# Optimization experiments

Measured on AMD Instinct MI355X. Metric: run time of the kernel, lower is better.

Reference implementation:

```python
import jax, jax.numpy as jnp
import numpy as np

NUM_HEADS = 16  # CLIP ViT-L num_attention_heads


def setup_inputs() -> dict:
    key = jax.random.key(0)
    ks = jax.random.split(key, 11)
    B, T, E = 16, 577, 1024
    d = {
        "hidden_states": jax.random.normal(ks[0], (B, T, E), jnp.float32),
        # token 'size' from prior merging steps; sizes are >= 1 in practice
        "size": jax.random.uniform(ks[1], (B, T), jnp.float32) + 1.0,
        "wq": jax.random.normal(ks[2], (E, E), jnp.float32) * (E ** -0.5),
        "bq": jax.random.normal(ks[3], (E,), jnp.float32) * 0.02,
        "wk": jax.random.normal(ks[4], (E, E), jnp.float32) * (E ** -0.5),
        "bk": jax.random.normal(ks[5], (E,), jnp.float32) * 0.02,
        "wv": jax.random.normal(ks[6], (E, E), jnp.float32) * (E ** -0.5),
        "bv": jax.random.normal(ks[7], (E,), jnp.float32) * 0.02,
        "wo": jax.random.normal(ks[8], (E, E), jnp.float32) * (E ** -0.5),
        "bo": jax.random.normal(ks[9], (E,), jnp.float32) * 0.02,
    }
    return d


def reference(hidden_states, size, wq, bq, wk, bk, wv, bv, wo, bo):
    B, T, E = hidden_states.shape
    H = NUM_HEADS
    D = E // H
    scale = D ** -0.5

    # torch nn.Linear: y = x @ W.T + b
    q = (hidden_states @ wq.T + bq) * scale
    k = hidden_states @ wk.T + bk
    v = hidden_states @ wv.T + bv

    def split_heads(x):  # [B,T,E] -> [B,H,T,D]
        return x.reshape(B, T, H, D).transpose(0, 2, 1, 3)

    qh, kh, vh = split_heads(q), split_heads(k), split_heads(v)

    # raw logits (before size bias), [B,H,T,T]
    attn_logits = jnp.einsum("bhtd,bhsd->bhts", qh, kh)

    # att_score: mean over the flattened bsz*num_heads dim, on raw logits
    att_score = attn_logits.mean(axis=(0, 1))  # [T,T]

    # additive log-size bias over keys
    attn_logits = attn_logits + jnp.log(size)[:, None, None, :]

    probs = jax.nn.softmax(attn_logits, axis=-1)  # dropout p=0 / eval
    out = jnp.einsum("bhts,bhsd->bhtd", probs, vh)
    out = out.transpose(0, 2, 1, 3).reshape(B, T, E)
    attn_output = out @ wo.T + bo

    # mean over heads of key states: [B,T,D]
    mean_keys = kh.mean(axis=1)

    return attn_output, mean_keys, att_score
```

## Files before the change

kernel.cpp:

```cpp
#include <hip/hip_runtime.h>
#include <hip/hip_bf16.h>
#include <math.h>

typedef __attribute__((ext_vector_type(8))) short s16x8;
typedef __attribute__((ext_vector_type(4))) short s16x4;
typedef __attribute__((ext_vector_type(4))) float f32x4;
typedef __attribute__((ext_vector_type(8))) __bf16 bf16x8;

#define MFMA16(a, b, c) __builtin_amdgcn_mfma_f32_16x16x32_bf16( \
    __builtin_bit_cast(bf16x8, (a)), __builtin_bit_cast(bf16x8, (b)), (c), 0, 0, 0)

__device__ __forceinline__ short f2b(float f) {
    __bf16 h = (__bf16)f;
    return __builtin_bit_cast(short, h);
}
__device__ __forceinline__ float b2f(short b) {
    union { unsigned u; float f; } x;
    x.u = ((unsigned)(unsigned short)b) << 16;
    return x.f;
}

__device__ __forceinline__ void gload16(const void* g, void* l) {
    __builtin_amdgcn_global_load_lds(
        (const __attribute__((address_space(1))) unsigned int*)g,
        (__attribute__((address_space(3))) unsigned int*)l, 16, 0, 0);
}

__global__ void k_f32_to_bf16(const float* __restrict__ in, short* __restrict__ out, long n) {
    long i = ((long)blockIdx.x * blockDim.x + threadIdx.x) * 4;
    long stride = (long)gridDim.x * blockDim.x * 4;
    for (; i < n; i += stride) {
        float4 v = *(const float4*)(in + i);
        s16x4 o = { f2b(v.x), f2b(v.y), f2b(v.z), f2b(v.w) };
        *(s16x4*)(out + i) = o;
    }
}

__global__ void k_wconv4(const float* __restrict__ w0, const float* __restrict__ w1,
                         const float* __restrict__ w2, const float* __restrict__ w3,
                         short* __restrict__ out, long n) {
    int wsel = blockIdx.y;
    const float* src = (wsel == 0) ? w0 : (wsel == 1) ? w1 : (wsel == 2) ? w2 : w3;
    short* dst = out + (long)wsel * n;
    long i = ((long)blockIdx.x * blockDim.x + threadIdx.x) * 4;
    if (i >= n) return;
    float4 v = *(const float4*)(src + i);
    s16x4 o = { f2b(v.x), f2b(v.y), f2b(v.z), f2b(v.w) };
    *(s16x4*)(dst + i) = o;
}

__global__ void k_sizepad(const float* __restrict__ size, float* __restrict__ out,
                          int B, int T, int SP) {
    int i = blockIdx.x * blockDim.x + threadIdx.x;
    if (i >= B * SP) return;
    int b = i / SP, s = i % SP;
    out[i] = (s < T) ? size[b * T + s] : 0.f;
}

template<bool ROUTE>
__global__ __launch_bounds__(256) void k_gemm4(
    const short* __restrict__ A, const short* __restrict__ Bw,
    const float* __restrict__ bb0, const float* __restrict__ bb1, const float* __restrict__ bb2,
    short* __restrict__ o0, short* __restrict__ o1, short* __restrict__ o2,
    float* __restrict__ Cf, int M, int N, int K, int Ntiles, float alpha0) {

    __shared__ short As[128 * 64];
    __shared__ short Bs[128 * 64];

    int nwg = gridDim.x, orig = blockIdx.x;
    int qq = nwg >> 3, rr = nwg & 7;
    int xcd = orig & 7, pos = orig >> 3;
    int wg = (xcd < rr ? xcd * (qq + 1) : rr * (qq + 1) + (xcd - rr) * qq) + pos;
    int bx = wg % Ntiles, by = wg / Ntiles;
    int row0 = by * 128, col0 = bx * 128;

    int tid = threadIdx.x;
    int lane = tid & 63, wave = tid >> 6;
    int wr = wave >> 1, wc = wave & 1;
    int lr = lane & 15, lg = lane >> 4;

    f32x4 acc[4][4];
    #pragma unroll
    for (int i = 0; i < 4; i++)
        #pragma unroll
        for (int j = 0; j < 4; j++)
            #pragma unroll
            for (int q = 0; q < 4; q++) acc[i][j][q] = 0.f;

    for (int k0 = 0; k0 < K; k0 += 64) {
        __syncthreads();
        #pragma unroll
        for (int i = 0; i < 4; ++i) {
            int cw = i * 256 + wave * 64;
            int c = cw + lane;
            int r = c >> 3;
            int cby = ((c & 7) * 16) ^ ((r & 7) << 4);
            int ra = row0 + r; ra = ra < M ? ra : M - 1;
            gload16((const char*)(A + (long)ra * K + k0) + cby, &As[cw * 8]);
            int rb = col0 + r; rb = rb < N ? rb : N - 1;
            gload16((const char*)(Bw + (long)rb * K + k0) + cby, &Bs[cw * 8]);
        }
        __syncthreads();
        #pragma unroll
        for (int ks = 0; ks < 2; ++ks) {
            s16x8 af[4], bfr[4];
            #pragma unroll
            for (int i = 0; i < 4; ++i) {
                int r = wr * 64 + i * 16 + lr;
                af[i] = *(const s16x8*)((const char*)As + r * 128 +
                        (((ks << 6) + (lg << 4)) ^ ((r & 7) << 4)));
            }
            #pragma unroll
            for (int j = 0; j < 4; ++j) {
                int r = wc * 64 + j * 16 + lr;
                bfr[j] = *(const s16x8*)((const char*)Bs + r * 128 +
                         (((ks << 6) + (lg << 4)) ^ ((r & 7) << 4)));
            }
            #pragma unroll
            for (int i = 0; i < 4; ++i)
                #pragma unroll
                for (int j = 0; j < 4; ++j)
                    acc[i][j] = MFMA16(af[i], bfr[j], acc[i][j]);
        }
    }

    #pragma unroll
    for (int i = 0; i < 4; i++) {
        int grow0 = row0 + wr * 64 + i * 16 + lg * 4;
        #pragma unroll
        for (int j = 0; j < 4; j++) {
            int gc = col0 + wc * 64 + j * 16 + lr;
            if (gc >= N) continue;
            if (ROUTE) {
                int which = gc >> 10, lc = gc & 1023;
                float bias = (which == 0 ? bb0 : which == 1 ? bb1 : bb2)[lc];
                float alpha = (which == 0) ? alpha0 : 1.0f;
                short* op = (which == 0 ? o0 : which == 1 ? o1 : o2);
                #pragma unroll
                for (int q = 0; q < 4; ++q) {
                    int r2 = grow0 + q;
                    if (r2 < M) op[(long)r2 * 1024 + lc] = f2b((acc[i][j][q] + bias) * alpha);
                }
            } else {
                float bias = bb0[gc];
                #pragma unroll
                for (int q = 0; q < 4; ++q) {
                    int r2 = grow0 + q;
                    if (r2 < M) Cf[(long)r2 * N + gc] = acc[i][j][q] + bias;
                }
            }
        }
    }
}

__device__ __forceinline__ void gemm_core(
    const short* __restrict__ Ab, const short* __restrict__ Bb,
    float* __restrict__ Cf, int M, int N, int K, int ldc, int row0, int col0) {
    __shared__ short As[128 * 64];
    __shared__ short Bs[128 * 64];
    int tid = threadIdx.x;
    int lane = tid & 63, wave = tid >> 6;
    int wr = wave >> 1, wc = wave & 1;
    int lr = lane & 15, lg = lane >> 4;
    f32x4 acc[4][4];
    #pragma unroll
    for (int i = 0; i < 4; i++)
        #pragma unroll
        for (int j = 0; j < 4; j++)
            #pragma unroll
            for (int q = 0; q < 4; q++) acc[i][j][q] = 0.f;

    for (int k0 = 0; k0 < K; k0 += 64) {
        __syncthreads();
        #pragma unroll
        for (int i = 0; i < 4; ++i) {
            int cw = i * 256 + wave * 64;
            int c = cw + lane;
            int r = c >> 3;
            int cby = ((c & 7) * 16) ^ ((r & 7) << 4);
            int ra = row0 + r; ra = ra < M ? ra : M - 1;
            gload16((const char*)(Ab + (long)ra * K + k0) + cby, &As[cw * 8]);
            int rb = col0 + r; rb = rb < N ? rb : N - 1;
            gload16((const char*)(Bb + (long)rb * K + k0) + cby, &Bs[cw * 8]);
        }
        __syncthreads();
        #pragma unroll
        for (int ks = 0; ks < 2; ++ks) {
            s16x8 af[4], bfr[4];
            #pragma unroll
            for (int i = 0; i < 4; ++i) {
                int r = wr * 64 + i * 16 + lr;
                af[i] = *(const s16x8*)((const char*)As + r * 128 +
                        (((ks << 6) + (lg << 4)) ^ ((r & 7) << 4)));
            }
            #pragma unroll
            for (int j = 0; j < 4; ++j) {
                int r = wc * 64 + j * 16 + lr;
                bfr[j] = *(const s16x8*)((const char*)Bs + r * 128 +
                         (((ks << 6) + (lg << 4)) ^ ((r & 7) << 4)));
            }
            #pragma unroll
            for (int i = 0; i < 4; ++i)
                #pragma unroll
                for (int j = 0; j < 4; ++j)
                    acc[i][j] = MFMA16(af[i], bfr[j], acc[i][j]);
        }
    }
    #pragma unroll
    for (int i = 0; i < 4; i++) {
        int rbase = row0 + wr * 64 + i * 16 + lg * 4;
        #pragma unroll
        for (int j = 0; j < 4; j++) {
            int c = col0 + wc * 64 + j * 16 + lr;
            if (c >= N) continue;
            #pragma unroll
            for (int q = 0; q < 4; q++) {
                int r = rbase + q;
                if (r >= M) continue;
                Cf[(long)r * ldc + c] = acc[i][j][q];
            }
        }
    }
}

__global__ __launch_bounds__(256) void k_att(
    const short* __restrict__ q, const short* __restrict__ k,
    float* __restrict__ attp, int T, int E) {
    int z = blockIdx.z;
    gemm_core(q + (long)z * T * E, k + (long)z * T * E,
              attp + (long)z * T * T, T, T, E, T,
              blockIdx.y * 128, blockIdx.x * 128);
}

__global__ void k_mean_keys8(const short* __restrict__ Kb, float* __restrict__ out, int BT) {
    int i = blockIdx.x * blockDim.x + threadIdx.x;
    if (i >= BT * 8) return;
    int bt = i >> 3, d0 = (i & 7) * 8;
    const short* p = Kb + (long)bt * 1024 + d0;
    float s[8] = {0.f, 0.f, 0.f, 0.f, 0.f, 0.f, 0.f, 0.f};
    #pragma unroll
    for (int h = 0; h < 16; ++h) {
        s16x8 v = *(const s16x8*)(p + h * 64);
        #pragma unroll
        for (int j = 0; j < 8; ++j) s[j] += b2f(v[j]);
    }
    float4 o0 = {s[0] * 0.0625f, s[1] * 0.0625f, s[2] * 0.0625f, s[3] * 0.0625f};
    float4 o1 = {s[4] * 0.0625f, s[5] * 0.0625f, s[6] * 0.0625f, s[7] * 0.0625f};
    *(float4*)(out + (long)bt * 64 + d0) = o0;
    *(float4*)(out + (long)bt * 64 + d0 + 4) = o1;
}

__global__ void k_att_reduce(const float* __restrict__ part, float* __restrict__ out,
                             int n, int nb, long stride) {
    int i = blockIdx.x * blockDim.x + threadIdx.x;
    if (i >= n) return;
    float s = 0.f;
    for (int b = 0; b < nb; ++b) s += part[(long)b * stride + i];
    out[i] = s * 0.002707606174062286f;
}

__global__ __launch_bounds__(256) void k_vtrans(const short* __restrict__ v, short* __restrict__ vt,
                                                int B, int T, int H, int TP) {
    int b = blockIdx.z, h = blockIdx.y, t0 = blockIdx.x * 64;
    __shared__ short Vs[64][68];
    int tid = threadIdx.x;
    for (int c = tid; c < 512; c += 256) {
        int r = c >> 3, m = c & 7;
        s16x8 val = {0,0,0,0,0,0,0,0};
        if (t0 + r < T) val = *(const s16x8*)(v + ((long)(b * T + t0 + r)) * (H * 64) + h * 64 + m * 8);
        *(s16x8*)&Vs[r][m * 8] = val;
    }
    __syncthreads();
    for (int c = tid; c < 512; c += 256) {
        int d = c >> 3, mw = c & 7;
        s16x8 o;
        #pragma unroll
        for (int j = 0; j < 8; j++) o[j] = Vs[mw * 8 + j][d];
        *(s16x8*)(vt + ((long)((b * H + h) * 64 + d)) * TP + t0 + mw * 8) = o;
    }
}

__global__ __launch_bounds__(256) void k_flash(
    const short* __restrict__ Q, const short* __restrict__ Kb, const short* __restrict__ VT,
    const float* __restrict__ szp, short* __restrict__ Ctx,
    int B, int T, int E, int H, int SP, int TP, int NTQ) {
    int nwg = gridDim.x;
    int cpx = nwg >> 3;
    int wg = (blockIdx.x & 7) * cpx + (blockIdx.x >> 3);
    int tq = wg % NTQ, h = (wg / NTQ) % H, b = wg / (NTQ * H);
    int t0 = tq * 128;

    __shared__ short Ks[64][68];
    __shared__ short Vt[64][68];
    __shared__ short Ps[4][32][68];
    __shared__ float Ls[64];
    int tid = threadIdx.x, wid = tid >> 6, lane = tid & 63;
    int lr = lane & 15, lg = lane >> 4;

    s16x8 aqf[2][2];
    #pragma unroll
    for (int i = 0; i < 2; ++i) {
        int t = t0 + wid * 32 + i * 16 + lr; t = t < T ? t : T - 1;
        #pragma unroll
        for (int ks = 0; ks < 2; ++ks)
            aqf[i][ks] = *(const s16x8*)(Q + ((long)b * T + t) * E + h * 64 + ks * 32 + lg * 8);
    }

    const short* kb  = Kb + (long)b * T * E + h * 64;
    const short* vtb = VT + ((long)(b * H + h)) * 64 * TP;

    int c0 = tid, c1 = tid + 256;
    int r0 = c0 >> 3, m0 = c0 & 7, r1 = c1 >> 3, m1 = c1 & 7;
    s16x8 kreg0, kreg1, vreg0, vreg1;
    float lreg = 0.f;

    {
        int s = r0; s = s < T ? s : T - 1;
        kreg0 = *(const s16x8*)(kb + (long)s * E + m0 * 8);
        s = r1; s = s < T ? s : T - 1;
        kreg1 = *(const s16x8*)(kb + (long)s * E + m1 * 8);
        vreg0 = *(const s16x8*)(vtb + (long)r0 * TP + 0 + m0 * 8);
        vreg1 = *(const s16x8*)(vtb + (long)r1 * TP + 0 + m1 * 8);
        if (tid < 64) lreg = szp[b * SP + 0 + tid];
    }

    float mreg[2][4], lsum[2][4];
    f32x4 o[2][4];
    #pragma unroll
    for (int i = 0; i < 2; i++)
        #pragma unroll
        for (int q = 0; q < 4; q++) { mreg[i][q] = -INFINITY; lsum[i][q] = 0.f; }
    #pragma unroll
    for (int i = 0; i < 2; i++)
        #pragma unroll
        for (int jd = 0; jd < 4; jd++)
            #pragma unroll
            for (int q = 0; q < 4; q++) o[i][jd][q] = 0.f;

    for (int s0 = 0; s0 < T; s0 += 64) {
        *(s16x8*)&Ks[r0][m0 * 8] = kreg0;
        *(s16x8*)&Ks[r1][m1 * 8] = kreg1;
        *(s16x8*)&Vt[r0][m0 * 8] = vreg0;
        *(s16x8*)&Vt[r1][m1 * 8] = vreg1;
        if (tid < 64) Ls[tid] = lreg;
        __syncthreads();

        if (s0 + 64 < T) {
            int sn = s0 + 64;
            int s = sn + r0; s = s < T ? s : T - 1;
            kreg0 = *(const s16x8*)(kb + (long)s * E + m0 * 8);
            s = sn + r1; s = s < T ? s : T - 1;
            kreg1 = *(const s16x8*)(kb + (long)s * E + m1 * 8);
            vreg0 = *(const s16x8*)(vtb + (long)r0 * TP + sn + m0 * 8);
            vreg1 = *(const s16x8*)(vtb + (long)r1 * TP + sn + m1 * 8);
            if (tid < 64) lreg = szp[b * SP + sn + tid];
        }

        float szv[4];
        #pragma unroll
        for (int j = 0; j < 4; j++) szv[j] = Ls[j * 16 + lr];

        s16x8 kf[2][4];
        #pragma unroll
        for (int ks = 0; ks < 2; ++ks)
            #pragma unroll
            for (int j = 0; j < 4; ++j)
                kf[ks][j] = *(const s16x8*)&Ks[j * 16 + lr][ks * 32 + lg * 8];

        #pragma unroll
        for (int i = 0; i < 2; ++i) {
            f32x4 sf[4];
            #pragma unroll
            for (int j = 0; j < 4; j++)
                #pragma unroll
                for (int q = 0; q < 4; q++) sf[j][q] = 0.f;
            __builtin_amdgcn_s_setprio(1);
            #pragma unroll
            for (int ks = 0; ks < 2; ++ks)
                #pragma unroll
                for (int j = 0; j < 4; j++) sf[j] = MFMA16(aqf[i][ks], kf[ks][j], sf[j]);
            __builtin_amdgcn_s_setprio(0);

            float tmax[4];
            #pragma unroll
            for (int q = 0; q < 4; q++)
                tmax[q] = fmaxf(fmaxf(sf[0][q], sf[1][q]), fmaxf(sf[2][q], sf[3][q]));
            int ok = 1;
            #pragma unroll
            for (int q = 0; q < 4; q++) ok &= (tmax[q] <= mreg[i][q] + 11.0f) ? 1 : 0;
            if (!__all(ok)) {
                #pragma unroll
                for (int q = 0; q < 4; q++) {
                    #pragma unroll
                    for (int msk = 1; msk < 16; msk <<= 1)
                        tmax[q] = fmaxf(tmax[q], __shfl_xor(tmax[q], msk));
                    float mn = fmaxf(mreg[i][q], tmax[q]);
                    float al = exp2f(mreg[i][q] - mn);
                    mreg[i][q] = mn;
                    lsum[i][q] *= al;
                    #pragma unroll
                    for (int jd = 0; jd < 4; jd++) o[i][jd][q] *= al;
                }
            }
            float rs[4] = {0.f, 0.f, 0.f, 0.f};
            #pragma unroll
            for (int j = 0; j < 4; j++) {
                float szj = szv[j];
                #pragma unroll
                for (int q = 0; q < 4; q++) {
                    float p = exp2f(sf[j][q] - mreg[i][q]) * szj;
                    sf[j][q] = p;
                    rs[q] += p;
                }
            }
            #pragma unroll
            for (int q = 0; q < 4; q++) lsum[i][q] += rs[q];

            #pragma unroll
            for (int j = 0; j < 4; j++)
                #pragma unroll
                for (int q = 0; q < 4; q++)
                    Ps[wid][i * 16 + lg * 4 + q][j * 16 + lr] = f2b(sf[j][q]);

            __builtin_amdgcn_s_setprio(1);
            #pragma unroll
            for (int ks = 0; ks < 2; ++ks) {
                s16x8 ap = *(const s16x8*)&Ps[wid][i * 16 + lr][ks * 32 + lg * 8];
                #pragma unroll
                for (int jd = 0; jd < 4; jd++) {
                    s16x8 bv = *(const s16x8*)&Vt[jd * 16 + lr][ks * 32 + lg * 8];
                    o[i][jd] = MFMA16(ap, bv, o[i][jd]);
                }
            }
            __builtin_amdgcn_s_setprio(0);
        }
        __syncthreads();
    }

    short* cb = Ctx + ((long)b * T + t0) * E + h * 64;
    #pragma unroll
    for (int i = 0; i < 2; i++)
        #pragma unroll
        for (int q = 0; q < 4; q++) {
            float s = lsum[i][q];
            s += __shfl_xor(s, 1); s += __shfl_xor(s, 2);
            s += __shfl_xor(s, 4); s += __shfl_xor(s, 8);
            int t = wid * 32 + i * 16 + lg * 4 + q;
            if (t0 + t >= T) continue;
            float inv = 1.f / s;
            #pragma unroll
            for (int jd = 0; jd < 4; jd++)
                cb[(long)t * E + jd * 16 + lr] = f2b(o[i][jd][q] * inv);
        }
}

extern "C" void kernel_launch(void* const* d_in, const int* in_sizes, int n_in,
                              void* d_out, int out_size, void* d_ws, size_t ws_size,
                              hipStream_t stream) {
    (void)in_sizes; (void)n_in; (void)out_size; (void)ws_size;
    const int B = 16, T = 577, E = 1024, H = 16;
    const int SP = 640, TP = 640;
    const float* hs   = (const float*)d_in[0];
    const float* size = (const float*)d_in[1];
    const float* wq   = (const float*)d_in[2];
    const float* bq   = (const float*)d_in[3];
    const float* wk   = (const float*)d_in[4];
    const float* bk   = (const float*)d_in[5];
    const float* wv   = (const float*)d_in[6];
    const float* bv   = (const float*)d_in[7];
    const float* wo   = (const float*)d_in[8];
    const float* bo   = (const float*)d_in[9];

    float* out_attn = (float*)d_out;
    float* out_mk   = out_attn + (long)B * T * E;
    float* out_as   = out_mk + (long)B * T * 64;

    long nBTE = (long)B * T * E;
    long nEE  = (long)E * E;
    char* ws = (char*)d_ws;
    short* hs_b  = (short*)ws; ws += nBTE * 2;
    short* wq_b  = (short*)ws; ws += nEE * 2;
    short* wk_b  = (short*)ws; ws += nEE * 2;
    short* wv_b  = (short*)ws; ws += nEE * 2;
    short* wo_b  = (short*)ws; ws += nEE * 2;
    short* q_b   = (short*)ws; ws += nBTE * 2;
    short* k_b   = (short*)ws; ws += nBTE * 2;
    short* v_b   = (short*)ws; ws += nBTE * 2;
    short* ctx_b = (short*)ws; ws += nBTE * 2;
    float* szpad = (float*)ws; ws += (long)B * SP * 4;
    float* att_p = (float*)ws; ws += (long)B * T * T * 4;
    short* vt = (short*)att_p;

    k_f32_to_bf16<<<2048, 256, 0, stream>>>(hs, hs_b, nBTE);
    {
        dim3 gw((nEE / 4 + 255) / 256, 4);
        k_wconv4<<<gw, 256, 0, stream>>>(wq, wk, wv, wo, wq_b, nEE);
    }
    k_sizepad<<<(B * SP + 255) / 256, 256, 0, stream>>>(size, szpad, B, T, SP);

    int M = B * T;
    {
        int Mtiles = (M + 127) / 128, Ntiles = 3072 / 128;
        k_gemm4<true><<<Mtiles * Ntiles, 256, 0, stream>>>(
            hs_b, wq_b, bq, bk, bv, q_b, k_b, v_b, nullptr, M, 3072, E, Ntiles,
            0.18033688011112042f);
    }

    dim3 g_att((T + 127) / 128, (T + 127) / 128, B);
    k_att<<<g_att, dim3(256), 0, stream>>>(q_b, k_b, att_p, T, E);
    k_att_reduce<<<((T * T) + 255) / 256, 256, 0, stream>>>(att_p, out_as, T * T, B, (long)T * T);

    dim3 g_vt((T + 63) / 64, H, B);
    k_vtrans<<<g_vt, dim3(256), 0, stream>>>(v_b, vt, B, T, H, TP);

    k_mean_keys8<<<((B * T * 8) + 255) / 256, 256, 0, stream>>>(k_b, out_mk, B * T);

    const int NTQ = (T + 127) / 128;
    int nfl = NTQ * H * B;
    k_flash<<<nfl, dim3(256), 0, stream>>>(q_b, k_b, vt, szpad, ctx_b, B, T, E, H, SP, TP, NTQ);

    {
        int Mtiles = (M + 127) / 128, Ntiles = 1024 / 128;
        k_gemm4<false><<<Mtiles * Ntiles, 256, 0, stream>>>(
            ctx_b, wo_b, bo, nullptr, nullptr, nullptr, nullptr, nullptr,
            out_attn, M, 1024, E, Ntiles, 1.0f);
    }
}
```

Before: 295.2 us.

## Double-buffer LDS tiles in GEMM and attention-score kernels to overlap loads

Replaces the single-buffered load/sync/compute loop in the projection GEMM and the batched q·k score kernel with a shared double-buffered core. The next K-tile's global-to-LDS loads are issued before computing on the current tile, and global pointers are precomputed and advanced. MFMA sections are wrapped in s_setprio to favour matrix issue. This doubles LDS use per block to 64 KB, which may reduce occupancy, and adds a trailing barrier per iteration.

```diff
diff --git a/kernel.cpp b/kernel.cpp
--- a/kernel.cpp
+++ b/kernel.cpp
@@ -57,6 +57,87 @@
     out[i] = (s < T) ? size[b * T + s] : 0.f;
 }
 
+__device__ __forceinline__ void core_dbuf(
+    const short* __restrict__ A, const short* __restrict__ Bw,
+    int M, int N, int K, int row0, int col0,
+    short* As, short* Bs,
+    f32x4 acc[4][4]) {
+    int tid = threadIdx.x;
+    int lane = tid & 63, wave = tid >> 6;
+    int wr = wave >> 1, wc = wave & 1;
+    int lr = lane & 15, lg = lane >> 4;
+
+    const char* ga[4]; const char* gb[4]; int ldo[4];
+    #pragma unroll
+    for (int i = 0; i < 4; ++i) {
+        int cw = i * 256 + wave * 64;
+        int c = cw + lane;
+        int r = c >> 3;
+        int cby = ((c & 7) * 16) ^ ((r & 7) << 4);
+        int ra = row0 + r; ra = ra < M ? ra : M - 1;
+        int rb = col0 + r; rb = rb < N ? rb : N - 1;
+        ga[i] = (const char*)(A + (long)ra * K) + cby;
+        gb[i] = (const char*)(Bw + (long)rb * K) + cby;
+        ldo[i] = cw * 8;
+    }
+    #pragma unroll
+    for (int i = 0; i < 4; i++)
+        #pragma unroll
+        for (int j = 0; j < 4; j++)
+            #pragma unroll
+            for (int q = 0; q < 4; q++) acc[i][j][q] = 0.f;
+
+    #pragma unroll
+    for (int i = 0; i < 4; ++i) {
+        gload16(ga[i], As + ldo[i]);
+        gload16(gb[i], Bs + ldo[i]);
+        ga[i] += 128; gb[i] += 128;
+    }
+
+    int nt = K >> 6;
+    for (int t = 0; t < nt; ++t) {
+        int cur = t & 1;
+        asm volatile("s_waitcnt vmcnt(0)" ::: "memory");
+        __builtin_amdgcn_s_barrier();
+        if (t + 1 < nt) {
+            short* Ad = As + (cur ^ 1) * 8192;
+            short* Bd = Bs + (cur ^ 1) * 8192;
+            #pragma unroll
+            for (int i = 0; i < 4; ++i) {
+                gload16(ga[i], Ad + ldo[i]);
+                gload16(gb[i], Bd + ldo[i]);
+                ga[i] += 128; gb[i] += 128;
+            }
+        }
+        const short* Ab2 = As + cur * 8192;
+        const short* Bb2 = Bs + cur * 8192;
+        #pragma unroll
+        for (int ks = 0; ks < 2; ++ks) {
+            s16x8 af[4], bfr[4];
+            #pragma unroll
+            for (int i = 0; i < 4; ++i) {
+                int r = wr * 64 + i * 16 + lr;
+                af[i] = *(const s16x8*)((const char*)Ab2 + r * 128 +
+                        (((ks << 6) + (lg << 4)) ^ ((r & 7) << 4)));
+            }
+            #pragma unroll
+            for (int j = 0; j < 4; ++j) {
+                int r = wc * 64 + j * 16 + lr;
+                bfr[j] = *(const s16x8*)((const char*)Bb2 + r * 128 +
+                         (((ks << 6) + (lg << 4)) ^ ((r & 7) << 4)));
+            }
+            __builtin_amdgcn_s_setprio(1);
+            #pragma unroll
+            for (int i = 0; i < 4; ++i)
+                #pragma unroll
+                for (int j = 0; j < 4; ++j)
+                    acc[i][j] = MFMA16(af[i], bfr[j], acc[i][j]);
+            __builtin_amdgcn_s_setprio(0);
+        }
+        __builtin_amdgcn_s_barrier();
+    }
+}
+
 template<bool ROUTE>
 __global__ __launch_bounds__(256) void k_gemm4(
     const short* __restrict__ A, const short* __restrict__ Bw,
@@ -64,8 +145,8 @@
     short* __restrict__ o0, short* __restrict__ o1, short* __restrict__ o2,
     float* __restrict__ Cf, int M, int N, int K, int Ntiles, float alpha0) {
 
-    __shared__ short As[128 * 64];
-    __shared__ short Bs[128 * 64];
+    __shared__ short AS[2][128 * 64];
+    __shared__ short BS[2][128 * 64];
 
     int nwg = gridDim.x, orig = blockIdx.x;
     int qq = nwg >> 3, rr = nwg & 7;
@@ -80,49 +161,7 @@
     int lr = lane & 15, lg = lane >> 4;
 
     f32x4 acc[4][4];
-    #pragma unroll
-    for (int i = 0; i < 4; i++)
-        #pragma unroll
-        for (int j = 0; j < 4; j++)
-            #pragma unroll
-            for (int q = 0; q < 4; q++) acc[i][j][q] = 0.f;
-
-    for (int k0 = 0; k0 < K; k0 += 64) {
-        __syncthreads();
-        #pragma unroll
-        for (int i = 0; i < 4; ++i) {
-            int cw = i * 256 + wave * 64;
-            int c = cw + lane;
-            int r = c >> 3;
-            int cby = ((c & 7) * 16) ^ ((r & 7) << 4);
-            int ra = row0 + r; ra = ra < M ? ra : M - 1;
-            gload16((const char*)(A + (long)ra * K + k0) + cby, &As[cw * 8]);
-            int rb = col0 + r; rb = rb < N ? rb : N - 1;
-            gload16((const char*)(Bw + (long)rb * K + k0) + cby, &Bs[cw * 8]);
-        }
-        __syncthreads();
-        #pragma unroll
-        for (int ks = 0; ks < 2; ++ks) {
-            s16x8 af[4], bfr[4];
-            #pragma unroll
-            for (int i = 0; i < 4; ++i) {
-                int r = wr * 64 + i * 16 + lr;
-                af[i] = *(const s16x8*)((const char*)As + r * 128 +
-                        (((ks << 6) + (lg << 4)) ^ ((r & 7) << 4)));
-            }
-            #pragma unroll
-            for (int j = 0; j < 4; ++j) {
-                int r = wc * 64 + j * 16 + lr;
-                bfr[j] = *(const s16x8*)((const char*)Bs + r * 128 +
-                         (((ks << 6) + (lg << 4)) ^ ((r & 7) << 4)));
-            }
-            #pragma unroll
-            for (int i = 0; i < 4; ++i)
-                #pragma unroll
-                for (int j = 0; j < 4; ++j)
-                    acc[i][j] = MFMA16(af[i], bfr[j], acc[i][j]);
-        }
-    }
+    core_dbuf(A, Bw, M, N, K, row0, col0, &AS[0][0], &BS[0][0], acc);
 
     #pragma unroll
     for (int i = 0; i < 4; i++) {
@@ -153,83 +192,40 @@
     }
 }
 
-__device__ __forceinline__ void gemm_core(
-    const short* __restrict__ Ab, const short* __restrict__ Bb,
-    float* __restrict__ Cf, int M, int N, int K, int ldc, int row0, int col0) {
-    __shared__ short As[128 * 64];
-    __shared__ short Bs[128 * 64];
+__global__ __launch_bounds__(256) void k_att(
+    const short* __restrict__ q, const short* __restrict__ k,
+    float* __restrict__ attp, int T, int E) {
+    __shared__ short AS[2][128 * 64];
+    __shared__ short BS[2][128 * 64];
+    int z = blockIdx.z;
+    const short* Ab = q + (long)z * T * E;
+    const short* Bb = k + (long)z * T * E;
+    float* Cf = attp + (long)z * T * T;
+    int row0 = blockIdx.y * 128, col0 = blockIdx.x * 128;
+
     int tid = threadIdx.x;
     int lane = tid & 63, wave = tid >> 6;
     int wr = wave >> 1, wc = wave & 1;
     int lr = lane & 15, lg = lane >> 4;
+
     f32x4 acc[4][4];
-    #pragma unroll
-    for (int i = 0; i < 4; i++)
-        #pragma unroll
-        for (int j = 0; j < 4; j++)
-            #pragma unroll
-            for (int q = 0; q < 4; q++) acc[i][j][q] = 0.f;
-
-    for (int k0 = 0; k0 < K; k0 += 64) {
-        __syncthreads();
-        #pragma unroll
-        for (int i = 0; i < 4; ++i) {
-            int cw = i * 256 + wave * 64;
-            int c = cw + lane;
-            int r = c >> 3;
-            int cby = ((c & 7) * 16) ^ ((r & 7) << 4);
-            int ra = row0 + r; ra = ra < M ? ra : M - 1;
-            gload16((const char*)(Ab + (long)ra * K + k0) + cby, &As[cw * 8]);
-            int rb = col0 + r; rb = rb < N ? rb : N - 1;
-            gload16((const char*)(Bb + (long)rb * K + k0) + cby, &Bs[cw * 8]);
-        }
-        __syncthreads();
-        #pragma unroll
-        for (int ks = 0; ks < 2; ++ks) {
-            s16x8 af[4], bfr[4];
-            #pragma unroll
-            for (int i = 0; i < 4; ++i) {
-                int r = wr * 64 + i * 16 + lr;
-                af[i] = *(const s16x8*)((const char*)As + r * 128 +
-                        (((ks << 6) + (lg << 4)) ^ ((r & 7) << 4)));
-            }
-            #pragma unroll
-            for (int j = 0; j < 4; ++j) {
-                int r = wc * 64 + j * 16 + lr;
-                bfr[j] = *(const s16x8*)((const char*)Bs + r * 128 +
-                         (((ks << 6) + (lg << 4)) ^ ((r & 7) << 4)));
-            }
-            #pragma unroll
-            for (int i = 0; i < 4; ++i)
-                #pragma unroll
-                for (int j = 0; j < 4; ++j)
-                    acc[i][j] = MFMA16(af[i], bfr[j], acc[i][j]);
-        }
-    }
+    core_dbuf(Ab, Bb, T, T, E, row0, col0, &AS[0][0], &BS[0][0], acc);
+
     #pragma unroll
     for (int i = 0; i < 4; i++) {
         int rbase = row0 + wr * 64 + i * 16 + lg * 4;
         #pragma unroll
         for (int j = 0; j < 4; j++) {
             int c = col0 + wc * 64 + j * 16 + lr;
-            if (c >= N) continue;
+            if (c >= T) continue;
             #pragma unroll
             for (int q = 0; q < 4; q++) {
                 int r = rbase + q;
-                if (r >= M) continue;
-                Cf[(long)r * ldc + c] = acc[i][j][q];
-            }
-        }
-    }
-}
-
-__global__ __launch_bounds__(256) void k_att(
-    const short* __restrict__ q, const short* __restrict__ k,
-    float* __restrict__ attp, int T, int E) {
-    int z = blockIdx.z;
-    gemm_core(q + (long)z * T * E, k + (long)z * T * E,
-              attp + (long)z * T * T, T, T, E, T,
-              blockIdx.y * 128, blockIdx.x * 128);
+                if (r >= T) continue;
+                Cf[(long)r * T + c] = acc[i][j][q];
+            }
+        }
+    }
 }
 
 __global__ void k_mean_keys8(const short* __restrict__ Kb, float* __restrict__ out, int BT) {
```

After: 309.3 us. +4.8%, slower.

## Fold size weights into V and compute softmax row sums via extra MFMA tile

Applied to the files above, without the earlier changes.

Pre-multiplies V by the per-key size weight during the transpose kernel, and appends a row of size values to the V tile in shared memory so the softmax denominator comes out of a fifth MFMA column block. This removes the per-element multiply by size and the scalar row-sum accumulation and shuffle reduction in the flash loop. In exchange it adds one more MFMA per step, more accumulator registers, and rounds both the scaled V and the size values to bf16, which can cost precision.

```diff
diff --git a/kernel.cpp b/kernel.cpp
--- a/kernel.cpp
+++ b/kernel.cpp
@@ -260,10 +260,13 @@
 }
 
 __global__ __launch_bounds__(256) void k_vtrans(const short* __restrict__ v, short* __restrict__ vt,
-                                                int B, int T, int H, int TP) {
+                                                const float* __restrict__ szp,
+                                                int B, int T, int H, int TP, int SP) {
     int b = blockIdx.z, h = blockIdx.y, t0 = blockIdx.x * 64;
     __shared__ short Vs[64][68];
+    __shared__ float Szs[64];
     int tid = threadIdx.x;
+    if (tid < 64) Szs[tid] = szp[b * SP + t0 + tid];
     for (int c = tid; c < 512; c += 256) {
         int r = c >> 3, m = c & 7;
         s16x8 val = {0,0,0,0,0,0,0,0};
@@ -275,7 +278,7 @@
         int d = c >> 3, mw = c & 7;
         s16x8 o;
         #pragma unroll
-        for (int j = 0; j < 8; j++) o[j] = Vs[mw * 8 + j][d];
+        for (int j = 0; j < 8; j++) o[j] = f2b(b2f(Vs[mw * 8 + j][d]) * Szs[mw * 8 + j]);
         *(s16x8*)(vt + ((long)((b * H + h) * 64 + d)) * TP + t0 + mw * 8) = o;
     }
 }
@@ -291,11 +294,12 @@
     int t0 = tq * 128;
 
     __shared__ short Ks[64][68];
-    __shared__ short Vt[64][68];
+    __shared__ short Vt[80][68];
     __shared__ short Ps[4][32][68];
-    __shared__ float Ls[64];
     int tid = threadIdx.x, wid = tid >> 6, lane = tid & 63;
     int lr = lane & 15, lg = lane >> 4;
+
+    for (int c = tid; c < 15 * 68; c += 256) Vt[65 + c / 68][c % 68] = 0;
 
     s16x8 aqf[2][2];
     #pragma unroll
@@ -312,7 +316,7 @@
     int c0 = tid, c1 = tid + 256;
     int r0 = c0 >> 3, m0 = c0 & 7, r1 = c1 >> 3, m1 = c1 & 7;
     s16x8 kreg0, kreg1, vreg0, vreg1;
-    float lreg = 0.f;
+    float szreg = 0.f;
 
     {
         int s = r0; s = s < T ? s : T - 1;
@@ -321,19 +325,19 @@
         kreg1 = *(const s16x8*)(kb + (long)s * E + m1 * 8);
         vreg0 = *(const s16x8*)(vtb + (long)r0 * TP + 0 + m0 * 8);
         vreg1 = *(const s16x8*)(vtb + (long)r1 * TP + 0 + m1 * 8);
-        if (tid < 64) lreg = szp[b * SP + 0 + tid];
-    }
-
-    float mreg[2][4], lsum[2][4];
-    f32x4 o[2][4];
+        if (tid < 64) szreg = szp[b * SP + 0 + tid];
+    }
+
+    float mreg[2][4];
+    f32x4 o[2][5];
     #pragma unroll
     for (int i = 0; i < 2; i++)
         #pragma unroll
-        for (int q = 0; q < 4; q++) { mreg[i][q] = -INFINITY; lsum[i][q] = 0.f; }
+        for (int q = 0; q < 4; q++) mreg[i][q] = -INFINITY;
     #pragma unroll
     for (int i = 0; i < 2; i++)
         #pragma unroll
-        for (int jd = 0; jd < 4; jd++)
+        for (int jd = 0; jd < 5; jd++)
             #pragma unroll
             for (int q = 0; q < 4; q++) o[i][jd][q] = 0.f;
 
@@ -342,7 +346,7 @@
         *(s16x8*)&Ks[r1][m1 * 8] = kreg1;
         *(s16x8*)&Vt[r0][m0 * 8] = vreg0;
         *(s16x8*)&Vt[r1][m1 * 8] = vreg1;
-        if (tid < 64) Ls[tid] = lreg;
+        if (tid < 64) Vt[64][tid] = f2b(szreg);
         __syncthreads();
 
         if (s0 + 64 < T) {
@@ -353,12 +357,8 @@
             kreg1 = *(const s16x8*)(kb + (long)s * E + m1 * 8);
             vreg0 = *(const s16x8*)(vtb + (long)r0 * TP + sn + m0 * 8);
             vreg1 = *(const s16x8*)(vtb + (long)r1 * TP + sn + m1 * 8);
-            if (tid < 64) lreg = szp[b * SP + sn + tid];
-        }
-
-        float szv[4];
-        #pragma unroll
-        for (int j = 0; j < 4; j++) szv[j] = Ls[j * 16 + lr];
+            if (tid < 64) szreg = szp[b * SP + sn + tid];
+        }
 
         s16x8 kf[2][4];
         #pragma unroll
@@ -397,37 +397,22 @@
                     float mn = fmaxf(mreg[i][q], tmax[q]);
                     float al = exp2f(mreg[i][q] - mn);
                     mreg[i][q] = mn;
-                    lsum[i][q] *= al;
                     #pragma unroll
-                    for (int jd = 0; jd < 4; jd++) o[i][jd][q] *= al;
+                    for (int jd = 0; jd < 5; jd++) o[i][jd][q] *= al;
                 }
             }
-            float rs[4] = {0.f, 0.f, 0.f, 0.f};
-            #pragma unroll
-            for (int j = 0; j < 4; j++) {
-                float szj = szv[j];
-                #pragma unroll
-                for (int q = 0; q < 4; q++) {
-                    float p = exp2f(sf[j][q] - mreg[i][q]) * szj;
-                    sf[j][q] = p;
-                    rs[q] += p;
-                }
-            }
-            #pragma unroll
-            for (int q = 0; q < 4; q++) lsum[i][q] += rs[q];
-
             #pragma unroll
             for (int j = 0; j < 4; j++)
                 #pragma unroll
                 for (int q = 0; q < 4; q++)
-                    Ps[wid][i * 16 + lg * 4 + q][j * 16 + lr] = f2b(sf[j][q]);
+                    Ps[wid][i * 16 + lg * 4 + q][j * 16 + lr] = f2b(exp2f(sf[j][q] - mreg[i][q]));
 
             __builtin_amdgcn_s_setprio(1);
             #pragma unroll
             for (int ks = 0; ks < 2; ++ks) {
                 s16x8 ap = *(const s16x8*)&Ps[wid][i * 16 + lr][ks * 32 + lg * 8];
                 #pragma unroll
-                for (int jd = 0; jd < 4; jd++) {
+                for (int jd = 0; jd < 5; jd++) {
                     s16x8 bv = *(const s16x8*)&Vt[jd * 16 + lr][ks * 32 + lg * 8];
                     o[i][jd] = MFMA16(ap, bv, o[i][jd]);
                 }
@@ -442,9 +427,7 @@
     for (int i = 0; i < 2; i++)
         #pragma unroll
         for (int q = 0; q < 4; q++) {
-            float s = lsum[i][q];
-            s += __shfl_xor(s, 1); s += __shfl_xor(s, 2);
-            s += __shfl_xor(s, 4); s += __shfl_xor(s, 8);
+            float s = __shfl(o[i][4][q], lane & 48);
             int t = wid * 32 + i * 16 + lg * 4 + q;
             if (t0 + t >= T) continue;
             float inv = 1.f / s;
@@ -511,7 +494,7 @@
     k_att_reduce<<<((T * T) + 255) / 256, 256, 0, stream>>>(att_p, out_as, T * T, B, (long)T * T);
 
     dim3 g_vt((T + 63) / 64, H, B);
-    k_vtrans<<<g_vt, dim3(256), 0, stream>>>(v_b, vt, B, T, H, TP);
+    k_vtrans<<<g_vt, dim3(256), 0, stream>>>(v_b, vt, szpad, B, T, H, TP, SP);
 
     k_mean_keys8<<<((B * T * 8) + 255) / 256, 256, 0, stream>>>(k_b, out_mk, B * T);
 
```

New measurement: 292.2 us. About the same (-1.0%).
